# Kernel tuning notes

Hardware: AMD Instinct MI355X
Metric: run time of the kernel (lower is better)

The kernel has to match this reference:

```python
import jax, jax.numpy as jnp
import numpy as np

BATCH, SEQ_LEN, NOISE_DIM, SEQ_DIM, HID = 8192, 256, 8, 4, 64

def setup_inputs() -> dict:
    key = jax.random.key(0)
    ks = jax.random.split(key, 6)
    s = lambda k, shp, fan: jax.random.normal(k, shp, jnp.float32) * (1.0 / np.sqrt(fan))
    return {
        "noise": jax.random.normal(ks[0], (BATCH, SEQ_LEN, NOISE_DIM), jnp.float32),
        "Wx": s(ks[1], (SEQ_DIM + NOISE_DIM, 4 * HID), SEQ_DIM + NOISE_DIM),
        "Wh": s(ks[2], (HID, 4 * HID), HID),
        "b": jnp.zeros((4 * HID,), jnp.float32),
        "W1": s(ks[3], (HID, HID), HID), "b1": jnp.zeros((HID,), jnp.float32),
        "W2": s(ks[4], (HID, HID), HID), "b2": jnp.zeros((HID,), jnp.float32),
        "W3": s(ks[5], (HID, SEQ_DIM), HID), "b3": jnp.zeros((SEQ_DIM,), jnp.float32),
    }

def reference(noise, Wx, Wh, b, W1, b1, W2, b2, W3, b3):
    batch = noise.shape[0]
    # log_series=True -> initial x is zeros
    x0 = jnp.zeros((batch, SEQ_DIM), noise.dtype)
    h0 = jnp.zeros((batch, HID), noise.dtype)
    c0 = jnp.zeros((batch, HID), noise.dtype)
    noise_t = jnp.swapaxes(noise[:, : SEQ_LEN - 1, :], 0, 1)  # [L-1, B, noise_dim]

    def step(carry, n_t):
        x, h, c = carry
        inp = jnp.concatenate([x, n_t], axis=-1)           # [B, seq_dim+noise_dim]
        z = inp @ Wx + h @ Wh + b                          # [B, 4H], keras gate order i,f,g,o
        i, f, g, o = jnp.split(z, 4, axis=-1)
        c = jax.nn.sigmoid(f) * c + jax.nn.sigmoid(i) * jnp.tanh(g)
        h = jax.nn.sigmoid(o) * jnp.tanh(c)
        y = jax.nn.relu(h @ W1 + b1)
        y = jax.nn.relu(y @ W2 + b2)
        x_new = y @ W3 + b3                                # [B, seq_dim]
        return (x_new, h, c), x_new

    _, xs = jax.lax.scan(step, (x0, h0, c0), noise_t)       # [L-1, B, seq_dim]
    seq = jnp.concatenate([x0[None], xs], axis=0)           # [L, B, seq_dim]
    seq = jnp.swapaxes(seq, 0, 1)                           # [B, L, seq_dim]
    return jnp.cumsum(seq, axis=1)
```

## Files before the change

kernel.cpp:

```cpp
#include <hip/hip_runtime.h>


typedef _Float16 h8 __attribute__((ext_vector_type(8)));
typedef __fp16 p2h __attribute__((ext_vector_type(2)));
typedef float f4 __attribute__((ext_vector_type(4)));

#define MFMA(a, b, c) __builtin_amdgcn_mfma_f32_16x16x32_f16(a, b, c, 0, 0, 0)

constexpr int SEQ = 256, STEPS = 255, ND = 8, SD = 4, HID = 64, G4 = 256;
constexpr int HST  = 72;
constexpr int A2ST = 24;

__device__ __forceinline__ void store4h(_Float16* p, f4 v) {
    p2h lo = __builtin_amdgcn_cvt_pkrtz(v[0], v[1]);
    p2h hi = __builtin_amdgcn_cvt_pkrtz(v[2], v[3]);
    float2 st;
    st.x = __builtin_bit_cast(float, lo);
    st.y = __builtin_bit_cast(float, hi);
    *(float2*)p = st;
}
__device__ __forceinline__ void store2h(_Float16* p, float a, float b_) {
    p2h v = __builtin_amdgcn_cvt_pkrtz(a, b_);
    *(float*)p = __builtin_bit_cast(float, v);
}

__global__ __launch_bounds__(256, 2) void genlstm_kernel(
    const float* __restrict__ noise, const float* __restrict__ Wx,
    const float* __restrict__ Wh, const float* __restrict__ b,
    const float* __restrict__ W1, const float* __restrict__ b1,
    const float* __restrict__ W2, const float* __restrict__ b2,
    const float* __restrict__ W3, const float* __restrict__ b3,
    float* __restrict__ out)
{
    __shared__ alignas(16) _Float16 Hb[2 * 16 * HST];
    __shared__ alignas(16) _Float16 Y1b[16 * HST];
    __shared__ alignas(16) _Float16 Y2b[16 * HST];
    __shared__ alignas(16) _Float16 A2b[4 * 16 * A2ST];
    __shared__ alignas(16) _Float16 Zb[8];

    const int tid = threadIdx.x, wid = tid >> 6, lane = tid & 63;
    const int col = lane & 15, quad = lane >> 4, q8 = quad * 8;
    const int row0 = blockIdx.x * 16;
    const int n0 = wid * 16 + col;
    const int wq = wid * 16 + quad * 4;

    h8 wg[4][3], w1f[2], w2f[2], w3f[2];
    #pragma unroll
    for (int g = 0; g < 4; ++g)
        #pragma unroll
        for (int s = 0; s < 3; ++s)
            #pragma unroll
            for (int j = 0; j < 8; ++j) {
                const int k = 32 * s + q8 + j;
                const int n = 64 * g + n0;
                float v;
                if (k < 64) v = Wh[k * G4 + n];
                else if (k < 76) v = Wx[(k - 64) * G4 + n];
                else v = 0.0f;
                wg[g][s][j] = (_Float16)v;
            }
    #pragma unroll
    for (int s = 0; s < 2; ++s)
        #pragma unroll
        for (int j = 0; j < 8; ++j) {
            const int k = 32 * s + q8 + j;
            w1f[s][j] = (_Float16)W1[k * HID + n0];
            w2f[s][j] = (_Float16)W2[k * HID + n0];
            w3f[s][j] = (_Float16)(col < 4 ? W3[k * SD + col] : 0.0f);
        }
    f4 bzv[4], b1v, b2v, b3v;
    #pragma unroll
    for (int r = 0; r < 4; ++r) {
        #pragma unroll
        for (int g = 0; g < 4; ++g) bzv[g][r] = b[64 * g + wq + r];
        b1v[r] = b1[wq + r];
        b2v[r] = b2[wq + r];
        b3v[r] = (quad == 0) ? b3[r] : 0.0f;
    }

    for (int i = tid; i < 2 * 16 * HST; i += 256) Hb[i] = (_Float16)0;
    for (int i = tid; i < 4 * 16 * A2ST; i += 256) A2b[i] = (_Float16)0;
    if (tid < 8) Zb[tid] = (_Float16)0;
    if (tid < 16) {
        float4 z; z.x = z.y = z.z = z.w = 0.0f;
        *(float4*)(out + (size_t)(row0 + tid) * SEQ * SD) = z;
    }
    __syncthreads();

    const int nrow = lane >> 2, ncc = (lane & 3) * 2;
    const float* nptr = noise + ((size_t)(row0 + nrow) * SEQ) * ND + ncc;
    _Float16* a2n = &A2b[(wid * 16 + nrow) * A2ST + 4 + ncc];
    _Float16* a2x = &A2b[(wid * 16 + col) * A2ST];
    const _Float16* a2rd = (quad < 2) ? &A2b[(wid * 16 + col) * A2ST + 8 * quad] : Zb;
    _Float16* Hrow[2] = { &Hb[col * HST], &Hb[(16 + col) * HST] };
    _Float16* Y1row = &Y1b[col * HST];
    _Float16* Y2row = &Y2b[col * HST];
    float* outp = out + ((size_t)(row0 + col) * SEQ + 1) * SD;

    {
        float2 nz = *(const float2*)nptr;
        store2h(a2n, nz.x, nz.y);
        nptr += ND;
    }

    f4 cst = {0.f, 0.f, 0.f, 0.f}, run = {0.f, 0.f, 0.f, 0.f};
    f4 zi = bzv[0], zf = bzv[1], zg = bzv[2], zo = bzv[3];
    h8 h0, h1;

    auto body = [&](int pb) {
        float2 nz = *(const float2*)nptr;
        nptr += ND;

        h8 a2 = *(const h8*)a2rd;
        zi = MFMA(wg[0][2], a2, zi);
        zf = MFMA(wg[1][2], a2, zf);
        zg = MFMA(wg[2][2], a2, zg);
        zo = MFMA(wg[3][2], a2, zo);

        f4 hv;
        #pragma unroll
        for (int r = 0; r < 4; ++r) {
            float Ei = __expf(-fmaxf(zi[r], -15.f));
            float Ef = __expf(-fmaxf(zf[r], -15.f));
            float Eg = __expf(-2.f * fmaxf(zg[r], -15.f));
            float Eo = __expf(-zo[r]);
            float Di = 1.f + Ei, Df = 1.f + Ef, Dg = 1.f + Eg, Do = 1.f + Eo;
            float DiDg = Di * Dg;
            float cn = (cst[r] * DiDg + (2.f - Dg) * Df) *
                       __builtin_amdgcn_rcpf(Df * DiDg);
            cst[r] = cn;
            float Ec = __expf(-2.f * fmaxf(cn, -15.f));
            hv[r] = (1.f - Ec) * __builtin_amdgcn_rcpf(Do * (1.f + Ec));
        }
        store4h(Hrow[pb ^ 1] + wq, hv);
        __syncthreads();

        const _Float16* hb = Hrow[pb ^ 1];
        h0 = *(const h8*)(hb + q8);
        h1 = *(const h8*)(hb + 32 + q8);
        f4 y1 = b1v;
        y1 = MFMA(w1f[0], h0, y1);
        y1 = MFMA(w1f[1], h1, y1);
        #pragma unroll
        for (int r = 0; r < 4; ++r) y1[r] = fmaxf(y1[r], 0.0f);
        store4h(Y1row + wq, y1);
        __syncthreads();

        h8 p0 = *(const h8*)(Y1row + q8);
        h8 p1 = *(const h8*)(Y1row + 32 + q8);
        f4 y2 = b2v;
        y2 = MFMA(w2f[0], p0, y2);
        y2 = MFMA(w2f[1], p1, y2);
        #pragma unroll
        for (int r = 0; r < 4; ++r) y2[r] = fmaxf(y2[r], 0.0f);
        store4h(Y2row + wq, y2);
        __syncthreads();

        h8 q0 = *(const h8*)(Y2row + q8);
        h8 q1 = *(const h8*)(Y2row + 32 + q8);
        f4 x = b3v;
        x = MFMA(w3f[0], q0, x);
        x = MFMA(w3f[1], q1, x);

        zi = bzv[0]; zi = MFMA(wg[0][0], h0, zi); zi = MFMA(wg[0][1], h1, zi);
        zf = bzv[1]; zf = MFMA(wg[1][0], h0, zf); zf = MFMA(wg[1][1], h1, zf);
        zg = bzv[2]; zg = MFMA(wg[2][0], h0, zg); zg = MFMA(wg[2][1], h1, zg);
        zo = bzv[3]; zo = MFMA(wg[3][0], h0, zo); zo = MFMA(wg[3][1], h1, zo);

        if (quad == 0) {
            store4h(a2x, x);
            if (wid == 0) {
                run += x;
                *(f4*)outp = run;
            }
        }
        store2h(a2n, nz.x, nz.y);
        outp += SD;
    };

    #pragma unroll 1
    for (int t = 0; t < STEPS - 1; t += 2) {
        body(0);
        body(1);
    }
    body(0);
}

extern "C" void kernel_launch(void* const* d_in, const int* in_sizes, int n_in,
                              void* d_out, int out_size, void* d_ws, size_t ws_size,
                              hipStream_t stream) {
    genlstm_kernel<<<512, 256, 0, stream>>>(
        (const float*)d_in[0], (const float*)d_in[1], (const float*)d_in[2],
        (const float*)d_in[3], (const float*)d_in[4], (const float*)d_in[5],
        (const float*)d_in[6], (const float*)d_in[7], (const float*)d_in[8],
        (const float*)d_in[9], (float*)d_out);
}
```

Baseline: 408.6 us.

## Fold output projection W3 into LSTM input weights to drop per-step sync stage

```diff
diff --git a/kernel.cpp b/kernel.cpp
--- a/kernel.cpp
+++ b/kernel.cpp
@@ -8,8 +8,7 @@
 #define MFMA(a, b, c) __builtin_amdgcn_mfma_f32_16x16x32_f16(a, b, c, 0, 0, 0)
 
 constexpr int SEQ = 256, STEPS = 255, ND = 8, SD = 4, HID = 64, G4 = 256;
-constexpr int HST  = 72;
-constexpr int A2ST = 24;
+constexpr int HST = 72;
 
 __device__ __forceinline__ void store4h(_Float16* p, f4 v) {
     p2h lo = __builtin_amdgcn_cvt_pkrtz(v[0], v[1]);
@@ -19,9 +18,13 @@
     st.y = __builtin_bit_cast(float, hi);
     *(float2*)p = st;
 }
-__device__ __forceinline__ void store2h(_Float16* p, float a, float b_) {
-    p2h v = __builtin_amdgcn_cvt_pkrtz(a, b_);
-    *(float*)p = __builtin_bit_cast(float, v);
+__device__ __forceinline__ h8 buildnf(float4 nv, int quad) {
+    f4 d = {0.f, 0.f, 0.f, 0.f};
+    if (quad < 2) {
+        d[0] = __builtin_bit_cast(float, __builtin_amdgcn_cvt_pkrtz(nv.x, nv.y));
+        d[1] = __builtin_bit_cast(float, __builtin_amdgcn_cvt_pkrtz(nv.z, nv.w));
+    }
+    return __builtin_bit_cast(h8, d);
 }
 
 __global__ __launch_bounds__(256, 2) void genlstm_kernel(
@@ -32,11 +35,9 @@
     const float* __restrict__ W3, const float* __restrict__ b3,
     float* __restrict__ out)
 {
-    __shared__ alignas(16) _Float16 Hb[2 * 16 * HST];
+    __shared__ alignas(16) _Float16 Hb[16 * HST];
     __shared__ alignas(16) _Float16 Y1b[16 * HST];
     __shared__ alignas(16) _Float16 Y2b[16 * HST];
-    __shared__ alignas(16) _Float16 A2b[4 * 16 * A2ST];
-    __shared__ alignas(16) _Float16 Zb[8];
 
     const int tid = threadIdx.x, wid = tid >> 6, lane = tid & 63;
     const int col = lane & 15, quad = lane >> 4, q8 = quad * 8;
@@ -44,21 +45,29 @@
     const int n0 = wid * 16 + col;
     const int wq = wid * 16 + quad * 4;
 
-    h8 wg[4][3], w1f[2], w2f[2], w3f[2];
+    h8 wh[4][2], wy[4][2], wgn[4], w1f[2], w2f[2], w3f[2];
     #pragma unroll
-    for (int g = 0; g < 4; ++g)
-        #pragma unroll
-        for (int s = 0; s < 3; ++s)
+    for (int g = 0; g < 4; ++g) {
+        const int n = 64 * g + n0;
+        #pragma unroll
+        for (int s = 0; s < 2; ++s)
             #pragma unroll
             for (int j = 0; j < 8; ++j) {
                 const int k = 32 * s + q8 + j;
-                const int n = 64 * g + n0;
-                float v;
-                if (k < 64) v = Wh[k * G4 + n];
-                else if (k < 76) v = Wx[(k - 64) * G4 + n];
-                else v = 0.0f;
-                wg[g][s][j] = (_Float16)v;
+                wh[g][s][j] = (_Float16)Wh[k * G4 + n];
+                float acc = 0.f;
+                #pragma unroll
+                for (int d = 0; d < 4; ++d) acc += W3[k * SD + d] * Wx[d * G4 + n];
+                wy[g][s][j] = (_Float16)acc;
             }
+        #pragma unroll
+        for (int j = 0; j < 8; ++j) {
+            float v = 0.f;
+            if (quad == 0 && j < 4) v = Wx[(4 + j) * G4 + n];
+            if (quad == 1 && j < 4) v = Wx[(8 + j) * G4 + n];
+            wgn[g][j] = (_Float16)v;
+        }
+    }
     #pragma unroll
     for (int s = 0; s < 2; ++s)
         #pragma unroll
@@ -72,51 +81,56 @@
     #pragma unroll
     for (int r = 0; r < 4; ++r) {
         #pragma unroll
-        for (int g = 0; g < 4; ++g) bzv[g][r] = b[64 * g + wq + r];
+        for (int g = 0; g < 4; ++g) {
+            float acc = b[64 * g + wq + r];
+            #pragma unroll
+            for (int d = 0; d < 4; ++d) acc += b3[d] * Wx[d * G4 + 64 * g + wq + r];
+            bzv[g][r] = acc;
+        }
         b1v[r] = b1[wq + r];
         b2v[r] = b2[wq + r];
         b3v[r] = (quad == 0) ? b3[r] : 0.0f;
     }
 
-    for (int i = tid; i < 2 * 16 * HST; i += 256) Hb[i] = (_Float16)0;
-    for (int i = tid; i < 4 * 16 * A2ST; i += 256) A2b[i] = (_Float16)0;
-    if (tid < 8) Zb[tid] = (_Float16)0;
+    for (int i = tid; i < 16 * HST; i += 256) {
+        Hb[i] = (_Float16)0; Y1b[i] = (_Float16)0; Y2b[i] = (_Float16)0;
+    }
     if (tid < 16) {
         float4 z; z.x = z.y = z.z = z.w = 0.0f;
         *(float4*)(out + (size_t)(row0 + tid) * SEQ * SD) = z;
     }
     __syncthreads();
 
-    const int nrow = lane >> 2, ncc = (lane & 3) * 2;
-    const float* nptr = noise + ((size_t)(row0 + nrow) * SEQ) * ND + ncc;
-    _Float16* a2n = &A2b[(wid * 16 + nrow) * A2ST + 4 + ncc];
-    _Float16* a2x = &A2b[(wid * 16 + col) * A2ST];
-    const _Float16* a2rd = (quad < 2) ? &A2b[(wid * 16 + col) * A2ST + 8 * quad] : Zb;
-    _Float16* Hrow[2] = { &Hb[col * HST], &Hb[(16 + col) * HST] };
+    _Float16* HbRow = &Hb[col * HST];
     _Float16* Y1row = &Y1b[col * HST];
     _Float16* Y2row = &Y2b[col * HST];
-    float* outp = out + ((size_t)(row0 + col) * SEQ + 1) * SD;
-
-    {
-        float2 nz = *(const float2*)nptr;
-        store2h(a2n, nz.x, nz.y);
-        nptr += ND;
-    }
+    const float* nqp = noise + ((size_t)(row0 + col) * SEQ) * ND + 4 * quad;
+    float* outp = out + ((size_t)(row0 + col) * SEQ) * SD;
+
+    float4 nv0;
+    if (quad < 2) nv0 = *(const float4*)nqp;
+    h8 nf = buildnf(nv0, quad);
 
     f4 cst = {0.f, 0.f, 0.f, 0.f}, run = {0.f, 0.f, 0.f, 0.f};
     f4 zi = bzv[0], zf = bzv[1], zg = bzv[2], zo = bzv[3];
-    h8 h0, h1;
-
-    auto body = [&](int pb) {
-        float2 nz = *(const float2*)nptr;
-        nptr += ND;
-
-        h8 a2 = *(const h8*)a2rd;
-        zi = MFMA(wg[0][2], a2, zi);
-        zf = MFMA(wg[1][2], a2, zf);
-        zg = MFMA(wg[2][2], a2, zg);
-        zo = MFMA(wg[3][2], a2, zo);
-
+    h8 y2f0, y2f1;
+
+    #pragma unroll 1
+    for (int k = 0; k < STEPS; ++k) {
+        float4 nv;
+        nqp += ND;
+        if (quad < 2) nv = *(const float4*)nqp;
+
+        zi = MFMA(wgn[0], nf, zi);
+        zf = MFMA(wgn[1], nf, zf);
+        zg = MFMA(wgn[2], nf, zg);
+        zo = MFMA(wgn[3], nf, zo);
+        y2f0 = *(const h8*)(Y2row + q8);
+        y2f1 = *(const h8*)(Y2row + 32 + q8);
+        zi = MFMA(wy[0][0], y2f0, zi); zi = MFMA(wy[0][1], y2f1, zi);
+        zf = MFMA(wy[1][0], y2f0, zf); zf = MFMA(wy[1][1], y2f1, zf);
+        zg = MFMA(wy[2][0], y2f0, zg); zg = MFMA(wy[2][1], y2f1, zg);
+        zo = MFMA(wy[3][0], y2f0, zo); zo = MFMA(wy[3][1], y2f1, zo);
         f4 hv;
         #pragma unroll
         for (int r = 0; r < 4; ++r) {
@@ -132,18 +146,28 @@
             float Ec = __expf(-2.f * fmaxf(cn, -15.f));
             hv[r] = (1.f - Ec) * __builtin_amdgcn_rcpf(Do * (1.f + Ec));
         }
-        store4h(Hrow[pb ^ 1] + wq, hv);
+        store4h(HbRow + wq, hv);
         __syncthreads();
 
-        const _Float16* hb = Hrow[pb ^ 1];
-        h0 = *(const h8*)(hb + q8);
-        h1 = *(const h8*)(hb + 32 + q8);
+        h8 h0 = *(const h8*)(HbRow + q8);
+        h8 h1 = *(const h8*)(HbRow + 32 + q8);
         f4 y1 = b1v;
         y1 = MFMA(w1f[0], h0, y1);
         y1 = MFMA(w1f[1], h1, y1);
+        f4 x = b3v;
+        x = MFMA(w3f[0], y2f0, x);
+        x = MFMA(w3f[1], y2f1, x);
+        zi = bzv[0]; zi = MFMA(wh[0][0], h0, zi); zi = MFMA(wh[0][1], h1, zi);
+        zf = bzv[1]; zf = MFMA(wh[1][0], h0, zf); zf = MFMA(wh[1][1], h1, zf);
+        zg = bzv[2]; zg = MFMA(wh[2][0], h0, zg); zg = MFMA(wh[2][1], h1, zg);
+        zo = bzv[3]; zo = MFMA(wh[3][0], h0, zo); zo = MFMA(wh[3][1], h1, zo);
         #pragma unroll
         for (int r = 0; r < 4; ++r) y1[r] = fmaxf(y1[r], 0.0f);
         store4h(Y1row + wq, y1);
+        if (k > 0 && wid == 0 && quad == 0) {
+            run += x;
+            *(f4*)(outp + (size_t)k * SD) = run;
+        }
         __syncthreads();
 
         h8 p0 = *(const h8*)(Y1row + q8);
@@ -154,36 +178,19 @@
         #pragma unroll
         for (int r = 0; r < 4; ++r) y2[r] = fmaxf(y2[r], 0.0f);
         store4h(Y2row + wq, y2);
+        nf = buildnf(nv, quad);
         __syncthreads();
-
-        h8 q0 = *(const h8*)(Y2row + q8);
-        h8 q1 = *(const h8*)(Y2row + 32 + q8);
-        f4 x = b3v;
-        x = MFMA(w3f[0], q0, x);
-        x = MFMA(w3f[1], q1, x);
-
-        zi = bzv[0]; zi = MFMA(wg[0][0], h0, zi); zi = MFMA(wg[0][1], h1, zi);
-        zf = bzv[1]; zf = MFMA(wg[1][0], h0, zf); zf = MFMA(wg[1][1], h1, zf);
-        zg = bzv[2]; zg = MFMA(wg[2][0], h0, zg); zg = MFMA(wg[2][1], h1, zg);
-        zo = bzv[3]; zo = MFMA(wg[3][0], h0, zo); zo = MFMA(wg[3][1], h1, zo);
-
-        if (quad == 0) {
-            store4h(a2x, x);
-            if (wid == 0) {
-                run += x;
-                *(f4*)outp = run;
-            }
-        }
-        store2h(a2n, nz.x, nz.y);
-        outp += SD;
-    };
-
-    #pragma unroll 1
-    for (int t = 0; t < STEPS - 1; t += 2) {
-        body(0);
-        body(1);
-    }
-    body(0);
+    }
+
+    y2f0 = *(const h8*)(Y2row + q8);
+    y2f1 = *(const h8*)(Y2row + 32 + q8);
+    f4 x = b3v;
+    x = MFMA(w3f[0], y2f0, x);
+    x = MFMA(w3f[1], y2f1, x);
+    if (wid == 0 && quad == 0) {
+        run += x;
+        *(f4*)(outp + (size_t)STEPS * SD) = run;
+    }
 }
 
 extern "C" void kernel_launch(void* const* d_in, const int* in_sizes, int n_in,
```

Result: slower. 487.5 us (+19.3%).
